# Performance work log

Measured on AMD Instinct MI355X. Metric: run time of the kernel, lower is better.

## Reference

```python
import jax, jax.numpy as jnp
import numpy as np

B, D = 16384, 512
NUM_CLASSES, K = 90, 32


def _l2norm(v, axis=-1):
    return v / jnp.sqrt(jnp.sum(v * v, axis=axis, keepdims=True) + 1e-12)


def setup_inputs() -> dict:
    key = jax.random.key(0)
    k1, k2, k3 = jax.random.split(key, 3)
    x = jax.random.normal(k1, (B, D), dtype=jnp.float32)
    labels = jax.random.randint(k2, (B,), 0, NUM_CLASSES, dtype=jnp.int64)
    centers = jax.random.normal(k3, (NUM_CLASSES, K, D), dtype=jnp.float32)
    return {"x": x, "labels": labels, "centers": centers}


def reference(x, labels, centers):
    # l2Norm applied to centers at init and to x in forward
    xn = _l2norm(x, axis=1)                       # [B, D]
    cn = _l2norm(centers, axis=-1)                # [C, K, D]
    c = cn[labels]                                # gather: [B, K, D]
    # dst_k = 1 - <x_b, center_{label_b, k}>
    dst = 1.0 - jnp.einsum("bd,bkd->bk", xn, c)   # [B, K]
    score = jax.nn.softmax(2.0 - dst, axis=1)     # softmax over K sub-centers
    per_sample = jnp.sum(score * dst, axis=1)     # [B]
    return jnp.mean(per_sample)                   # scalar loss
```

## Files before the change

kernel.cpp:

```cpp
#include <hip/hip_runtime.h>
#include <hip/hip_bf16.h>

#define BB 16384
#define DD 512
#define NCLS 90
#define KC 32
#define BUCKET 512
#define PRB 180
#define NSL 12

typedef __attribute__((ext_vector_type(8))) short short8;
typedef __attribute__((ext_vector_type(4))) float fx4;

static __device__ __forceinline__ short f2bf(float f) {
    unsigned u = __float_as_uint(f);
    unsigned r = (u + 0x7fffu + ((u >> 16) & 1u)) >> 16;
    return (short)r;
}
static __device__ __forceinline__ short8 pack8(float4 a, float4 b) {
    union { __hip_bfloat162 h[4]; short8 s; } u;
    u.h[0] = __float22bfloat162_rn(make_float2(a.x, a.y));
    u.h[1] = __float22bfloat162_rn(make_float2(a.z, a.w));
    u.h[2] = __float22bfloat162_rn(make_float2(b.x, b.y));
    u.h[3] = __float22bfloat162_rn(make_float2(b.z, b.w));
    return u.s;
}
static __device__ __forceinline__ void gload_lds16(const void* g, void* l) {
    __builtin_amdgcn_global_load_lds(
        (const __attribute__((address_space(1))) void*)g,
        (__attribute__((address_space(3))) void*)l, 16, 0, 0);
}

__global__ __launch_bounds__(1024)
void k_prep(const float* __restrict__ centers, const int* __restrict__ labels,
            short* __restrict__ cni, int* __restrict__ idx, int* __restrict__ cnt) {
    __shared__ int lab[BB];
    __shared__ int wcnt[16];

    int t = threadIdx.x, w = t >> 6, lane = t & 63;

    if ((int)blockIdx.x < PRB) {
        int row = blockIdx.x * 16 + w;
        const float4* p = (const float4*)(centers + (size_t)row * DD);
        float4 a = p[lane * 2];
        float4 b = p[lane * 2 + 1];
        float s = a.x * a.x + a.y * a.y + a.z * a.z + a.w * a.w
                + b.x * b.x + b.y * b.y + b.z * b.z + b.w * b.w;
#pragma unroll
        for (int m = 1; m < 64; m <<= 1) s += __shfl_xor(s, m, 64);
        float sc = rsqrtf(s + 1e-12f);
        short8 v;
        v[0] = f2bf(a.x * sc); v[1] = f2bf(a.y * sc);
        v[2] = f2bf(a.z * sc); v[3] = f2bf(a.w * sc);
        v[4] = f2bf(b.x * sc); v[5] = f2bf(b.y * sc);
        v[6] = f2bf(b.z * sc); v[7] = f2bf(b.w * sc);
        *(short8*)(cni + (size_t)row * DD + lane * 8) = v;
    } else {
        int c = blockIdx.x - PRB;
        for (int j = t; j < BB / 4; j += 1024)
            ((int4*)lab)[j] = ((const int4*)labels)[j];
        __syncthreads();

        int seg4 = w * (BB / 4 / 16);
        int cw = 0;
#pragma unroll
        for (int jj = 0; jj < 4; jj++) {
            int4 v = ((int4*)lab)[seg4 + jj * 64 + lane];
            cw += (v.x == c) + (v.y == c) + (v.z == c) + (v.w == c);
        }
#pragma unroll
        for (int m = 1; m < 64; m <<= 1) cw += __shfl_xor(cw, m, 64);
        if (lane == 0) wcnt[w] = cw;
        __syncthreads();
        int pos = c * BUCKET;
        for (int ww = 0; ww < w; ww++) pos += wcnt[ww];
#pragma unroll
        for (int jj = 0; jj < 4; jj++) {
            int4 v = ((int4*)lab)[seg4 + jj * 64 + lane];
            int gbase = (seg4 + jj * 64 + lane) * 4;
            { bool m = (v.x == c); unsigned long long k = __ballot(m);
              if (m) idx[pos + __popcll(k & ((1ull << lane) - 1ull))] = gbase;     pos += __popcll(k); }
            { bool m = (v.y == c); unsigned long long k = __ballot(m);
              if (m) idx[pos + __popcll(k & ((1ull << lane) - 1ull))] = gbase + 1; pos += __popcll(k); }
            { bool m = (v.z == c); unsigned long long k = __ballot(m);
              if (m) idx[pos + __popcll(k & ((1ull << lane) - 1ull))] = gbase + 2; pos += __popcll(k); }
            { bool m = (v.w == c); unsigned long long k = __ballot(m);
              if (m) idx[pos + __popcll(k & ((1ull << lane) - 1ull))] = gbase + 3; pos += __popcll(k); }
        }
        if (t == 0) {
            int s = 0;
#pragma unroll
            for (int i = 0; i < 16; i++) s += wcnt[i];
            cnt[c] = s;
        }
    }
}

__global__ __launch_bounds__(256, 2)
void k_main(const float* __restrict__ x,
            const short* __restrict__ cni,
            const int* __restrict__ cnt,
            const int* __restrict__ idx,
            float* __restrict__ partials) {
    __shared__ __align__(16) short c_lds[KC * DD];
    __shared__ __align__(16) float xf[16 * DD];
    __shared__ float S[2][16][34];
    __shared__ float xn2[2][16];
    __shared__ float red[256];

    int b = blockIdx.x;
    int c = b / NSL, p = b % NSL;
    int n = cnt[c];
    int nch = (n + 15) >> 4;
    int t = threadIdx.x, w = t >> 6, lane = t & 63;
    float loss = 0.f;

    if (p < nch) {
        const short* cbase = cni + (size_t)c * KC * DD;
#pragma unroll
        for (int it = 0; it < 8; it++) {
            int q = t + 256 * it;
            int drow = q >> 6, cc = q & 63;
            gload_lds16(cbase + drow * DD + (cc ^ (drow & 7)) * 8, &c_lds[q * 8]);
        }

        int r = lane & 15, g4 = lane >> 4;
        int kh = w >> 1, chf = w & 1;
        int nrow = (chf << 4) + r;
        int srow = t >> 4, l16 = t & 15;

        for (int ch = p; ch < nch; ch += NSL) {
            int off = ch << 4;
            int rem = n - off;

            int gi = 0;
            if (lane < 4) {
                int i = off + (w << 2) + lane; if (i > n - 1) i = n - 1;
                gi = idx[c * BUCKET + i];
            }
#pragma unroll
            for (int j = 0; j < 4; j++) {
                int row = (w << 2) + j;
                int g = __shfl(gi, j, 64);
                const char* src = (const char*)(x + (size_t)g * DD);
                int sl = (lane ^ (row & 7)) << 4;
                gload_lds16(src + sl,        &xf[row * DD]);
                gload_lds16(src + 1024 + sl, &xf[row * DD + 256]);
            }
            __syncthreads();

            fx4 acc = {0.f, 0.f, 0.f, 0.f};
            float nrm = 0.f;
#pragma unroll
            for (int ks = 0; ks < 8; ks++) {
                int cq = (kh * 8 + ks) * 4 + g4;
                int p0 = (2 * cq) ^ (r & 7);
                int p1 = (2 * cq + 1) ^ (r & 7);
                float4 a0 = *(const float4*)&xf[r * DD + p0 * 4];
                float4 a1 = *(const float4*)&xf[r * DD + p1 * 4];
                nrm += a0.x * a0.x + a0.y * a0.y + a0.z * a0.z + a0.w * a0.w
                     + a1.x * a1.x + a1.y * a1.y + a1.z * a1.z + a1.w * a1.w;
                short8 av = pack8(a0, a1);
                short8 bv = *(const short8*)&c_lds[nrow * DD + ((cq ^ (nrow & 7)) << 3)];
                acc = __builtin_amdgcn_mfma_f32_16x16x32_bf16(av, bv, acc, 0, 0, 0);
            }
            nrm += __shfl_xor(nrm, 16, 64);
            nrm += __shfl_xor(nrm, 32, 64);
            if (chf == 0 && g4 == 0) xn2[kh][r] = nrm;
#pragma unroll
            for (int j = 0; j < 4; j++)
                S[kh][(g4 << 2) + j][(chf << 4) + r] = acc[j];
            __syncthreads();

            {
                float xv = rsqrtf(xn2[0][srow] + xn2[1][srow] + 1e-12f);
                int c0 = l16 * 2;
                float sa = (S[0][srow][c0]     + S[1][srow][c0])     * xv;
                float sb = (S[0][srow][c0 + 1] + S[1][srow][c0 + 1]) * xv;
                float mx = fmaxf(sa, sb);
#pragma unroll
                for (int m = 1; m < 16; m <<= 1) mx = fmaxf(mx, __shfl_xor(mx, m, 64));
                float ea = expf(sa - mx), eb = expf(sb - mx);
                float Z = ea + eb;
                float num = ea * (1.f - sa) + eb * (1.f - sb);
#pragma unroll
                for (int m = 1; m < 16; m <<= 1) {
                    Z   += __shfl_xor(Z, m, 64);
                    num += __shfl_xor(num, m, 64);
                }
                if (l16 == 0 && srow < rem) loss += num / Z;
            }
        }
    }

    red[t] = loss;
    __syncthreads();
    for (int h = 128; h > 0; h >>= 1) {
        if (t < h) red[t] += red[t + h];
        __syncthreads();
    }
    if (t == 0) partials[b] = red[0];
}

__global__ void k_final(const float* __restrict__ partials, float* __restrict__ out) {
    __shared__ float red[256];
    int t = threadIdx.x;
    float s = 0.f;
    for (int i = t; i < NCLS * NSL; i += 256) s += partials[i];
    red[t] = s;
    __syncthreads();
    for (int h = 128; h > 0; h >>= 1) {
        if (t < h) red[t] += red[t + h];
        __syncthreads();
    }
    if (t == 0) out[0] = red[0] * (1.0f / (float)BB);
}

extern "C" void kernel_launch(void* const* d_in, const int* in_sizes, int n_in,
                              void* d_out, int out_size, void* d_ws, size_t ws_size,
                              hipStream_t stream) {
    const float* x       = (const float*)d_in[0];
    const int*   labels  = (const int*)d_in[1];
    const float* centers = (const float*)d_in[2];
    float* out = (float*)d_out;

    char* ws = (char*)d_ws;
    short* cni      = (short*)(ws + 0);
    int*   idx      = (int*)(ws + 3145728);
    int*   cnt      = (int*)(ws + 3407872);
    float* partials = (float*)(ws + 3473408);

    k_prep<<<PRB + NCLS, 1024, 0, stream>>>(centers, labels, cni, idx, cnt);
    k_main<<<NCLS * NSL, 256, 0, stream>>>(x, cni, cnt, idx, partials);
    k_final<<<1, 256, 0, stream>>>(partials, out);
}
```

Measured before the change: 29.81 us.

## Fuse final reduction via atomic counter, convert x to bf16 during load

Removes the separate final-reduction kernel by having the last-finishing main block sum the partials, using an atomic counter reset in the prep kernel. x rows are loaded into registers, their norms computed once, and they are stored to LDS as bf16, which halves LDS use and allows three blocks per CU. The softmax max-subtraction is dropped because cosine scores are bounded, and the per-class slice count is cut from 12 to 8. In exchange, async global-to-LDS loads are replaced with synchronous register loads and each block handles more chunks.

Result: slower. 44.05 us (+47.8%).

```diff
diff --git a/kernel.cpp b/kernel.cpp
--- a/kernel.cpp
+++ b/kernel.cpp
@@ -7,7 +7,7 @@
 #define KC 32
 #define BUCKET 512
 #define PRB 180
-#define NSL 12
+#define NP 8
 
 typedef __attribute__((ext_vector_type(8))) short short8;
 typedef __attribute__((ext_vector_type(4))) float fx4;
@@ -33,7 +33,8 @@
 
 __global__ __launch_bounds__(1024)
 void k_prep(const float* __restrict__ centers, const int* __restrict__ labels,
-            short* __restrict__ cni, int* __restrict__ idx, int* __restrict__ cnt) {
+            short* __restrict__ cni, int* __restrict__ idx, int* __restrict__ cnt,
+            int* __restrict__ counter) {
     __shared__ int lab[BB];
     __shared__ int wcnt[16];
 
@@ -57,6 +58,7 @@
         *(short8*)(cni + (size_t)row * DD + lane * 8) = v;
     } else {
         int c = blockIdx.x - PRB;
+        if (c == 0 && t == 0) *counter = 0;
         for (int j = t; j < BB / 4; j += 1024)
             ((int4*)lab)[j] = ((const int4*)labels)[j];
         __syncthreads();
@@ -96,24 +98,27 @@
     }
 }
 
-__global__ __launch_bounds__(256, 2)
-void k_main(const float* __restrict__ x,
-            const short* __restrict__ cni,
-            const int* __restrict__ cnt,
-            const int* __restrict__ idx,
-            float* __restrict__ partials) {
+__launch_bounds__(256, 3)
+__global__ void k_main(const float* __restrict__ x,
+                       const short* __restrict__ cni,
+                       const int* __restrict__ cnt,
+                       const int* __restrict__ idx,
+                       float* __restrict__ partials,
+                       int* __restrict__ counter,
+                       float* __restrict__ out) {
     __shared__ __align__(16) short c_lds[KC * DD];
-    __shared__ __align__(16) float xf[16 * DD];
+    __shared__ __align__(16) short x_lds[16 * DD];
     __shared__ float S[2][16][34];
-    __shared__ float xn2[2][16];
-    __shared__ float red[256];
+    __shared__ float xinv[16];
+    __shared__ float red4[4];
+    __shared__ int lastflag;
 
     int b = blockIdx.x;
-    int c = b / NSL, p = b % NSL;
+    int c = b >> 3, p = b & 7;
     int n = cnt[c];
     int nch = (n + 15) >> 4;
     int t = threadIdx.x, w = t >> 6, lane = t & 63;
-    float loss = 0.f;
+    float loss_acc = 0.f;
 
     if (p < nch) {
         const short* cbase = cni + (size_t)c * KC * DD;
@@ -124,63 +129,60 @@
             gload_lds16(cbase + drow * DD + (cc ^ (drow & 7)) * 8, &c_lds[q * 8]);
         }
 
+        int base = c * BUCKET;
+        int row16 = t >> 4, l16 = t & 15;
         int r = lane & 15, g4 = lane >> 4;
         int kh = w >> 1, chf = w & 1;
-        int nrow = (chf << 4) + r;
-        int srow = t >> 4, l16 = t & 15;
-
-        for (int ch = p; ch < nch; ch += NSL) {
+        int brow = (chf << 4) + r;
+
+        for (int ch = p; ch < nch; ch += NP) {
             int off = ch << 4;
             int rem = n - off;
 
-            int gi = 0;
-            if (lane < 4) {
-                int i = off + (w << 2) + lane; if (i > n - 1) i = n - 1;
-                gi = idx[c * BUCKET + i];
-            }
-#pragma unroll
-            for (int j = 0; j < 4; j++) {
-                int row = (w << 2) + j;
-                int g = __shfl(gi, j, 64);
-                const char* src = (const char*)(x + (size_t)g * DD);
-                int sl = (lane ^ (row & 7)) << 4;
-                gload_lds16(src + sl,        &xf[row * DD]);
-                gload_lds16(src + 1024 + sl, &xf[row * DD + 256]);
+            {
+                int i = off + row16; if (i > n - 1) i = n - 1;
+                int g = idx[base + i];
+                const float4* src = (const float4*)(x + (size_t)g * DD);
+                float4 va[4], vb[4];
+#pragma unroll
+                for (int jj = 0; jj < 4; jj++) {
+                    va[jj] = src[2 * l16 + 32 * jj];
+                    vb[jj] = src[2 * l16 + 32 * jj + 1];
+                }
+                float nrm = 0.f;
+#pragma unroll
+                for (int jj = 0; jj < 4; jj++) {
+                    int cc = l16 + 16 * jj;
+                    float4 a = va[jj], b4 = vb[jj];
+                    nrm += a.x * a.x + a.y * a.y + a.z * a.z + a.w * a.w
+                         + b4.x * b4.x + b4.y * b4.y + b4.z * b4.z + b4.w * b4.w;
+                    *(short8*)&x_lds[row16 * DD + ((cc ^ (row16 & 7)) << 3)] = pack8(a, b4);
+                }
+#pragma unroll
+                for (int m = 1; m < 16; m <<= 1) nrm += __shfl_xor(nrm, m, 64);
+                if (l16 == 0) xinv[row16] = rsqrtf(nrm + 1e-12f);
             }
             __syncthreads();
 
             fx4 acc = {0.f, 0.f, 0.f, 0.f};
-            float nrm = 0.f;
 #pragma unroll
             for (int ks = 0; ks < 8; ks++) {
-                int cq = (kh * 8 + ks) * 4 + g4;
-                int p0 = (2 * cq) ^ (r & 7);
-                int p1 = (2 * cq + 1) ^ (r & 7);
-                float4 a0 = *(const float4*)&xf[r * DD + p0 * 4];
-                float4 a1 = *(const float4*)&xf[r * DD + p1 * 4];
-                nrm += a0.x * a0.x + a0.y * a0.y + a0.z * a0.z + a0.w * a0.w
-                     + a1.x * a1.x + a1.y * a1.y + a1.z * a1.z + a1.w * a1.w;
-                short8 av = pack8(a0, a1);
-                short8 bv = *(const short8*)&c_lds[nrow * DD + ((cq ^ (nrow & 7)) << 3)];
+                int c16a = kh * 32 + ks * 4 + g4;
+                short8 av = *(const short8*)&x_lds[r * DD + ((c16a ^ (r & 7)) << 3)];
+                short8 bv = *(const short8*)&c_lds[brow * DD + ((c16a ^ (brow & 7)) << 3)];
                 acc = __builtin_amdgcn_mfma_f32_16x16x32_bf16(av, bv, acc, 0, 0, 0);
             }
-            nrm += __shfl_xor(nrm, 16, 64);
-            nrm += __shfl_xor(nrm, 32, 64);
-            if (chf == 0 && g4 == 0) xn2[kh][r] = nrm;
 #pragma unroll
             for (int j = 0; j < 4; j++)
                 S[kh][(g4 << 2) + j][(chf << 4) + r] = acc[j];
             __syncthreads();
 
             {
-                float xv = rsqrtf(xn2[0][srow] + xn2[1][srow] + 1e-12f);
+                float xv = xinv[row16];
                 int c0 = l16 * 2;
-                float sa = (S[0][srow][c0]     + S[1][srow][c0])     * xv;
-                float sb = (S[0][srow][c0 + 1] + S[1][srow][c0 + 1]) * xv;
-                float mx = fmaxf(sa, sb);
-#pragma unroll
-                for (int m = 1; m < 16; m <<= 1) mx = fmaxf(mx, __shfl_xor(mx, m, 64));
-                float ea = expf(sa - mx), eb = expf(sb - mx);
+                float sa = (S[0][row16][c0]     + S[1][row16][c0])     * xv;
+                float sb = (S[0][row16][c0 + 1] + S[1][row16][c0 + 1]) * xv;
+                float ea = __expf(sa), eb = __expf(sb);
                 float Z = ea + eb;
                 float num = ea * (1.f - sa) + eb * (1.f - sb);
 #pragma unroll
@@ -188,32 +190,34 @@
                     Z   += __shfl_xor(Z, m, 64);
                     num += __shfl_xor(num, m, 64);
                 }
-                if (l16 == 0 && srow < rem) loss += num / Z;
+                if (l16 == 0 && row16 < rem) loss_acc += num / Z;
             }
-        }
-    }
-
-    red[t] = loss;
+            __syncthreads();
+        }
+    }
+
+#pragma unroll
+    for (int m = 1; m < 64; m <<= 1) loss_acc += __shfl_xor(loss_acc, m, 64);
+    if (lane == 0) red4[w] = loss_acc;
     __syncthreads();
-    for (int h = 128; h > 0; h >>= 1) {
-        if (t < h) red[t] += red[t + h];
+    if (t == 0) {
+        partials[b] = red4[0] + red4[1] + red4[2] + red4[3];
+        __threadfence();
+        int old = atomicAdd(counter, 1);
+        lastflag = (old == (int)gridDim.x - 1);
+    }
+    __syncthreads();
+    if (lastflag) {
+        __threadfence();
+        float s = 0.f;
+        for (int i = t; i < NCLS * NP; i += 256)
+            s += __hip_atomic_load(&partials[i], __ATOMIC_RELAXED, __HIP_MEMORY_SCOPE_AGENT);
+#pragma unroll
+        for (int m = 1; m < 64; m <<= 1) s += __shfl_xor(s, m, 64);
+        if (lane == 0) red4[w] = s;
         __syncthreads();
-    }
-    if (t == 0) partials[b] = red[0];
-}
-
-__global__ void k_final(const float* __restrict__ partials, float* __restrict__ out) {
-    __shared__ float red[256];
-    int t = threadIdx.x;
-    float s = 0.f;
-    for (int i = t; i < NCLS * NSL; i += 256) s += partials[i];
-    red[t] = s;
-    __syncthreads();
-    for (int h = 128; h > 0; h >>= 1) {
-        if (t < h) red[t] += red[t + h];
-        __syncthreads();
-    }
-    if (t == 0) out[0] = red[0] * (1.0f / (float)BB);
+        if (t == 0) out[0] = (red4[0] + red4[1] + red4[2] + red4[3]) * (1.0f / (float)BB);
+    }
 }
 
 extern "C" void kernel_launch(void* const* d_in, const int* in_sizes, int n_in,
@@ -228,9 +232,9 @@
     short* cni      = (short*)(ws + 0);
     int*   idx      = (int*)(ws + 3145728);
     int*   cnt      = (int*)(ws + 3407872);
+    int*   counter  = (int*)(ws + 3408384);
     float* partials = (float*)(ws + 3473408);
 
-    k_prep<<<PRB + NCLS, 1024, 0, stream>>>(centers, labels, cni, idx, cnt);
-    k_main<<<NCLS * NSL, 256, 0, stream>>>(x, cni, cnt, idx, partials);
-    k_final<<<1, 256, 0, stream>>>(partials, out);
-}
+    k_prep<<<PRB + NCLS, 1024, 0, stream>>>(centers, labels, cni, idx, cnt, counter);
+    k_main<<<NCLS * NP, 256, 0, stream>>>(x, cni, cnt, idx, partials, counter, out);
+}
```
